# Optimization experiments

Hardware: AMD Instinct MI355X
Metric: run time of the kernel (lower is better)

## Reference

```python
import jax, jax.numpy as jnp
import numpy as np

N_ATOMS = 100000
N_CHANNELS = 4
N_EDGES = 6400000
SMEARING = 1.0


def setup_inputs() -> dict:
    key = jax.random.key(0)
    k1, k2, k3 = jax.random.split(key, 3)
    charges = jax.random.normal(k1, (N_ATOMS, N_CHANNELS), dtype=jnp.float32)
    neighbor_indices = jax.random.randint(k2, (N_EDGES, 2), 0, N_ATOMS, dtype=jnp.int64)
    # physical distances strictly positive, typical cutoff-range values
    neighbor_distances = jax.random.uniform(k3, (N_EDGES,), dtype=jnp.float32,
                                            minval=0.5, maxval=6.0)
    return {"charges": charges,
            "neighbor_indices": neighbor_indices,
            "neighbor_distances": neighbor_distances}


def reference(charges, neighbor_indices, neighbor_distances):
    # Short-range Coulomb potential: erfc(r / (sqrt(2)*smearing)) / r
    pot_bare = jax.scipy.special.erfc(
        neighbor_distances / (jnp.sqrt(jnp.float32(2.0)) * SMEARING)
    ) / neighbor_distances  # [E]

    atom_is = neighbor_indices[:, 0]
    atom_js = neighbor_indices[:, 1]

    contrib_is = charges[atom_js] * pot_bare[:, None]  # [E, C]
    potential = jnp.zeros_like(charges).at[atom_is].add(contrib_is)
    # half neighbor list (full_neighbor_list=False): symmetrize
    contrib_js = charges[atom_is] * pot_bare[:, None]
    potential = potential.at[atom_js].add(contrib_js)
    return potential / 2
```

## Files before the change

kernel.cpp:

```cpp
#include <hip/hip_runtime.h>
#include <hip/hip_fp16.h>

#define BLOCK 1024
#define NB_BIN 960
#define KCONS 48
#define RPB (NB_BIN / KCONS)
#define TILE_ATOMS 10000
#define NTILES_MAX 10
#define WPS_MAX 112
#define WPS_PAD 113
#define FB_TILE_ATOMS 10000
#define FB_TILE_FLOATS (FB_TILE_ATOMS * 2)
#define CPX 3
#define CHUNKS 24
#define RSQRT2 0.70710678118654752440f

typedef float v2f __attribute__((ext_vector_type(2)));
typedef unsigned long long ull;

__device__ __forceinline__ void atomic_add2(float* p, float a, float b) {
#if __has_builtin(__builtin_amdgcn_global_atomic_fadd_v2f32)
    v2f v = {a, b};
    __builtin_amdgcn_global_atomic_fadd_v2f32((v2f*)p, v);
#else
    unsafeAtomicAdd(p + 0, a);
    unsafeAtomicAdd(p + 1, b);
#endif
}

__device__ __forceinline__ void agent_store64(ull* p, ull v) {
    __hip_atomic_store(p, v, __ATOMIC_RELAXED, __HIP_MEMORY_SCOPE_AGENT);
}
__device__ __forceinline__ void agent_store32(unsigned int* p, unsigned int v) {
    __hip_atomic_store(p, v, __ATOMIC_RELAXED, __HIP_MEMORY_SCOPE_AGENT);
}

__device__ __forceinline__ float pot_half(float d) {
    float x = d * RSQRT2;
    float t = __builtin_amdgcn_rcpf(fmaf(0.3275911f, x, 1.0f));
    float p = fmaf(t, 0.5307027145f, -0.7265760135f);
    p = fmaf(t, p, 0.7107068705f);
    p = fmaf(t, p, -0.142248368f);
    p = fmaf(t, p, 0.127414796f);
    p *= t;
    return p * __expf(-0.5f * d * d) * __builtin_amdgcn_rcpf(d);
}

__global__ void detect_idx64_kernel(const unsigned int* __restrict__ idx_u32,
                                    int* __restrict__ flag) {
    __shared__ int nonzero;
    if (threadIdx.x == 0) nonzero = 0;
    __syncthreads();
    unsigned int v = idx_u32[2 * (threadIdx.x +   0) + 1]
                   | idx_u32[2 * (threadIdx.x + 256) + 1]
                   | idx_u32[2 * (threadIdx.x + 512) + 1]
                   | idx_u32[2 * (threadIdx.x + 768) + 1];
    if (v != 0u) atomicAdd(&nonzero, 1);
    __syncthreads();
    if (threadIdx.x == 0) *flag = (nonzero == 0) ? 1 : 0;
}


__global__ __launch_bounds__(BLOCK) void bin_kernel(
    const float4* __restrict__ charges, const void* __restrict__ idx,
    const float* __restrict__ dist,
    ull* __restrict__ entries, unsigned int* __restrict__ counts,
    float* __restrict__ out, const int* __restrict__ flag64,
    int n_edges, int nwords, int wps, int cap, int ntiles, int nb)
{
    __shared__ ull maskA[NTILES_MAX][WPS_PAD];
    __shared__ ull maskB[NTILES_MAX][WPS_PAD];
    __shared__ unsigned short wbase[NTILES_MAX][WPS_PAD];
    bool f64 = (*flag64 != 0);
    int b    = blockIdx.x;
    int lane = threadIdx.x & 63;
    int wave = threadIdx.x >> 6;
    ull lt = (1ull << lane) - 1ull;

    for (int wl = wave; wl < wps; wl += BLOCK / 64) {
        int gw = b * wps + wl;
        int ta = -1, tb = -1;
        if (gw < nwords) {
            int e = gw * 64 + lane;
            if (e < n_edges) {
                int a, bb;
                if (f64) { longlong2 w = ((const longlong2*)idx)[e]; a = (int)w.x; bb = (int)w.y; }
                else     { int2      w = ((const int2*)idx)[e];      a = w.x;      bb = w.y; }
                ta = a / TILE_ATOMS; tb = bb / TILE_ATOMS;
            }
        }
        for (int T = 0; T < ntiles; ++T) {
            ull ma = __ballot(ta == T);
            ull mb = __ballot(tb == T);
            if (lane == 0) { maskA[T][wl] = ma; maskB[T][wl] = mb; }
        }
    }
    __syncthreads();

    if ((int)threadIdx.x < ntiles) {
        int T = threadIdx.x;
        unsigned base = 0;
        for (int wl = 0; wl < wps; ++wl) {
            wbase[T][wl] = (unsigned short)base;
            base += (unsigned)(__popcll(maskA[T][wl]) + __popcll(maskB[T][wl]));
        }
        agent_store32(&counts[(size_t)T * nb + b],
                      base < (unsigned)cap ? base : (unsigned)cap);
    }
    __syncthreads();

    for (int wl = wave; wl < wps; wl += BLOCK / 64) {
        int gw = b * wps + wl;
        if (gw >= nwords) continue;
        int e = gw * 64 + lane;
        int a = 0, bb = 0, ta = -1, tb = -1;
        float q = 0.f;
        if (e < n_edges) {
            if (f64) { longlong2 w = ((const longlong2*)idx)[e]; a = (int)w.x; bb = (int)w.y; }
            else     { int2      w = ((const int2*)idx)[e];      a = w.x;      bb = w.y; }
            ta = a / TILE_ATOMS; tb = bb / TILE_ATOMS;
            q = pot_half(dist[e]);
        }
        ull qb = (ull)__float_as_uint(q) << 32;
        if (ta >= 0) {
            unsigned slot = wbase[ta][wl] + (unsigned)__popcll(maskA[ta][wl] & lt);
            ull* reg = entries + ((size_t)ta * nb + b) * cap;
            if (slot < (unsigned)cap) {
                unsigned lo = (unsigned)(a - ta * TILE_ATOMS) | ((unsigned)bb << 14);
                agent_store64(&reg[slot], qb | lo);
            } else {
                float4 g = charges[bb];
                float* o = out + (size_t)a * 4;
                unsafeAtomicAdd(o + 0, g.x * q); unsafeAtomicAdd(o + 1, g.y * q);
                unsafeAtomicAdd(o + 2, g.z * q); unsafeAtomicAdd(o + 3, g.w * q);
            }
        }
        if (tb >= 0) {
            unsigned slot = wbase[tb][wl] + (unsigned)__popcll(maskA[tb][wl])
                          + (unsigned)__popcll(maskB[tb][wl] & lt);
            ull* reg = entries + ((size_t)tb * nb + b) * cap;
            if (slot < (unsigned)cap) {
                unsigned lo = (unsigned)(bb - tb * TILE_ATOMS) | ((unsigned)a << 14);
                agent_store64(&reg[slot], qb | lo);
            } else {
                float4 g = charges[a];
                float* o = out + (size_t)bb * 4;
                unsafeAtomicAdd(o + 0, g.x * q); unsafeAtomicAdd(o + 1, g.y * q);
                unsafeAtomicAdd(o + 2, g.z * q); unsafeAtomicAdd(o + 3, g.w * q);
            }
        }
    }
}

__global__ __launch_bounds__(BLOCK, 8) void consume_pk(
    const float4* __restrict__ charges,
    const ull* __restrict__ entries, const unsigned int* __restrict__ counts,
    ull* __restrict__ partials, int cap, int nb, unsigned capmagic)
{
    __shared__ __half2 ht[TILE_ATOMS * 2];
    __shared__ unsigned cnts[RPB];
    int k = blockIdx.x % KCONS;
    int t = blockIdx.x / KCONS;
    for (int i = threadIdx.x; i < TILE_ATOMS * 2; i += BLOCK)
        ((unsigned*)ht)[i] = 0u;
    for (int r = threadIdx.x; r < RPB; r += BLOCK)
        cnts[r] = counts[(size_t)t * nb + k * RPB + r];
    __syncthreads();

    const ull* base = entries + ((size_t)t * nb + (size_t)k * RPB) * cap;
    int total = RPB * cap;
    for (int i0 = (int)threadIdx.x * 2; i0 < total; i0 += BLOCK * 2) {
        ulonglong2 e2 = *(const ulonglong2*)(base + i0);
        int r   = (int)(((ull)(unsigned)i0 * capmagic) >> 32);
        int pos = i0 - r * cap;
        unsigned cnt = cnts[r];
        #define PROC(EV)                                                     \
            { unsigned lo = (unsigned)(EV);                                  \
              int rel = lo & 16383; int other = (int)(lo >> 14);             \
              float q = __uint_as_float((unsigned)((EV) >> 32));             \
              float4 g = charges[other];                                     \
              __half2 h01 = __floats2half2_rn(g.x * q, g.y * q);             \
              __half2 h23 = __floats2half2_rn(g.z * q, g.w * q);             \
              unsafeAtomicAdd(&ht[rel * 2 + 0], h01);                        \
              unsafeAtomicAdd(&ht[rel * 2 + 1], h23); }
        if ((unsigned)pos     < cnt) PROC(e2.x)
        if ((unsigned)(pos+1) < cnt) PROC(e2.y)
        #undef PROC
    }
    __syncthreads();

    ull* pb = partials + (size_t)blockIdx.x * TILE_ATOMS;
    for (int r = threadIdx.x; r < TILE_ATOMS; r += BLOCK) {
        __half2 x0 = ht[r * 2 + 0], x1 = ht[r * 2 + 1];
        unsigned b0 = *(unsigned*)&x0, b1 = *(unsigned*)&x1;
        agent_store64(&pb[r], (ull)b0 | ((ull)b1 << 32));
    }
}

__global__ __launch_bounds__(256) void reduce_kernel(
    const ull* __restrict__ partials, float* __restrict__ out, int n_atoms)
{
    int a = blockIdx.x * 256 + threadIdx.x;
    if (a >= n_atoms) return;
    int t   = a / TILE_ATOMS;
    int rel = a - t * TILE_ATOMS;
    const ull* base = partials + ((size_t)t * KCONS) * TILE_ATOMS + rel;
    float4 s = make_float4(0.f, 0.f, 0.f, 0.f);
    #pragma unroll
    for (int k = 0; k < KCONS; ++k) {
        ull v = base[(size_t)k * TILE_ATOMS];
        s.x += __half2float(__ushort_as_half((unsigned short)( v        & 0xffff)));
        s.y += __half2float(__ushort_as_half((unsigned short)((v >> 16) & 0xffff)));
        s.z += __half2float(__ushort_as_half((unsigned short)((v >> 32) & 0xffff)));
        s.w += __half2float(__ushort_as_half((unsigned short)( v >> 48)));
    }
    float* o = out + (size_t)a * 4;
    atomic_add2(o + 0, s.x, s.y);
    atomic_add2(o + 2, s.z, s.w);
}


template <bool F64>
__device__ __forceinline__ void scan_chunk(
    const void* __restrict__ idx, const float* __restrict__ dist,
    const float2* __restrict__ charges2, float* __restrict__ tile,
    int tbase, int h, int e0, int e1)
{
    int ec = e0 + ((e1 - e0) & ~3);
    for (int e4 = e0 + (int)threadIdx.x * 4; e4 < ec; e4 += BLOCK * 4) {
        int a[4], b[4];
        if (F64) {
            #pragma unroll
            for (int k = 0; k < 4; ++k) {
                longlong2 w = ((const longlong2*)idx)[e4 + k];
                a[k] = (int)w.x; b[k] = (int)w.y;
            }
        } else {
            int4 w01 = ((const int4*)idx)[(e4 >> 1) + 0];
            int4 w23 = ((const int4*)idx)[(e4 >> 1) + 1];
            a[0] = w01.x; b[0] = w01.y; a[1] = w01.z; b[1] = w01.w;
            a[2] = w23.x; b[2] = w23.y; a[3] = w23.z; b[3] = w23.w;
        }
        float4 dv = *(const float4*)(dist + e4);
        float d[4] = {dv.x, dv.y, dv.z, dv.w};
        float q[4];
        #pragma unroll
        for (int k = 0; k < 4; ++k) q[k] = pot_half(d[k]);
        #pragma unroll
        for (int k = 0; k < 4; ++k) {
            unsigned ri = (unsigned)(a[k] - tbase);
            unsigned rj = (unsigned)(b[k] - tbase);
            if (ri < FB_TILE_ATOMS) {
                float2 g = charges2[b[k] * 2 + h];
                atomicAdd(&tile[ri * 2 + 0], g.x * q[k]);
                atomicAdd(&tile[ri * 2 + 1], g.y * q[k]);
            }
            if (rj < FB_TILE_ATOMS) {
                float2 g = charges2[a[k] * 2 + h];
                atomicAdd(&tile[rj * 2 + 0], g.x * q[k]);
                atomicAdd(&tile[rj * 2 + 1], g.y * q[k]);
            }
        }
    }
    for (int e = ec + (int)threadIdx.x; e < e1; e += BLOCK) {
        int a, b;
        if (F64) { longlong2 w = ((const longlong2*)idx)[e]; a = (int)w.x; b = (int)w.y; }
        else     { int2      w = ((const int2*)idx)[e];      a = w.x;      b = w.y; }
        unsigned ri = (unsigned)(a - tbase), rj = (unsigned)(b - tbase);
        if (ri < FB_TILE_ATOMS || rj < FB_TILE_ATOMS) {
            float q = pot_half(dist[e]);
            if (ri < FB_TILE_ATOMS) {
                float2 g = charges2[b * 2 + h];
                atomicAdd(&tile[ri * 2 + 0], g.x * q);
                atomicAdd(&tile[ri * 2 + 1], g.y * q);
            }
            if (rj < FB_TILE_ATOMS) {
                float2 g = charges2[a * 2 + h];
                atomicAdd(&tile[rj * 2 + 0], g.x * q);
                atomicAdd(&tile[rj * 2 + 1], g.y * q);
            }
        }
    }
}

__global__ __launch_bounds__(BLOCK, 8) void fused_tile_kernel(
    const float2* __restrict__ charges2, const void* __restrict__ idx,
    const float* __restrict__ dist, float* __restrict__ out,
    const int* __restrict__ flag64,
    int n_edges, int n_atoms, int ntiles, int epc)
{
    __shared__ float tile[FB_TILE_FLOATS];
    int x   = blockIdx.x & 7;
    int m   = blockIdx.x >> 3;
    int nth = ntiles * 2;
    int cw  = m / nth;
    int rem = m - cw * nth;
    int t   = rem >> 1;
    int h   = rem & 1;
    int c   = x * CPX + cw;
    int tbase = t * FB_TILE_ATOMS;
    for (int i = threadIdx.x; i < FB_TILE_FLOATS; i += BLOCK) tile[i] = 0.f;
    bool f64 = (*flag64 != 0);
    __syncthreads();

    int e0 = c * epc;
    int e1 = min(n_edges, e0 + epc);
    if (e0 < e1) {
        if (f64) scan_chunk<true >(idx, dist, charges2, tile, tbase, h, e0, e1);
        else     scan_chunk<false>(idx, dist, charges2, tile, tbase, h, e0, e1);
    }
    __syncthreads();

    const float2* src = (const float2*)tile;
    for (int r = threadIdx.x; r < FB_TILE_ATOMS; r += BLOCK) {
        int a = tbase + r;
        if (a >= n_atoms) break;
        float2 v = src[r];
        if (v.x != 0.f || v.y != 0.f)
            atomic_add2(out + (size_t)a * 4 + h * 2, v.x, v.y);
    }
}


extern "C" void kernel_launch(void* const* d_in, const int* in_sizes, int n_in,
                              void* d_out, int out_size, void* d_ws, size_t ws_size,
                              hipStream_t stream) {
    const float4* charges  = (const float4*)d_in[0];
    const float2* charges2 = (const float2*)d_in[0];
    const void*   idx      = d_in[1];
    const float*  dist     = (const float*)d_in[2];
    int n_edges = in_sizes[2];
    int n_atoms = in_sizes[0] / 4;
    int* flag   = (int*)d_ws;

    const size_t CTRL = 1024;
    int nwords = (n_edges + 63) / 64;
    int wps    = (nwords + NB_BIN - 1) / NB_BIN;
    int ntiles = (n_atoms + TILE_ATOMS - 1) / TILE_ATOMS;
    int slice  = wps * 64;
    int cap    = ((slice * 2 / (ntiles > 0 ? ntiles : 1)) * 115 / 100 + 63)
                 & ~63;
    unsigned capmagic = (unsigned)((0x100000000ull + cap - 1) / (unsigned)cap);
    size_t nreg           = (size_t)ntiles * NB_BIN;
    size_t counts_bytes   = (nreg * sizeof(unsigned int) + 255) & ~(size_t)255;
    size_t entries_bytes  = nreg * (size_t)cap * 8ull;
    size_t partials_bytes = (size_t)ntiles * KCONS * TILE_ATOMS * 8ull;
    size_t needed = CTRL + counts_bytes + entries_bytes + partials_bytes;
    bool use_binned = (ws_size >= needed) && (ntiles <= NTILES_MAX) &&
                      (wps <= WPS_MAX) && (n_atoms <= (1 << 17)) &&
                      (slice * 2 < 65536);

    (void)hipMemsetAsync(d_out, 0, (size_t)out_size * sizeof(float), stream);
    detect_idx64_kernel<<<1, 256, 0, stream>>>((const unsigned int*)idx, flag);

    if (use_binned) {
        unsigned int* counts = (unsigned int*)((char*)d_ws + CTRL);
        ull* entries  = (ull*)((char*)d_ws + CTRL + counts_bytes);
        ull* partials = (ull*)((char*)d_ws + CTRL + counts_bytes + entries_bytes);
        bin_kernel<<<NB_BIN, BLOCK, 0, stream>>>(
            charges, idx, dist, entries, counts, (float*)d_out, flag,
            n_edges, nwords, wps, cap, ntiles, NB_BIN);
        consume_pk<<<ntiles * KCONS, BLOCK, 0, stream>>>(
            charges, entries, counts, partials, cap, NB_BIN, capmagic);
        reduce_kernel<<<(n_atoms + 255) / 256, 256, 0, stream>>>(
            partials, (float*)d_out, n_atoms);
    } else {
        int ntiles_fb = (n_atoms + FB_TILE_ATOMS - 1) / FB_TILE_ATOMS;
        int epc = (((n_edges + CHUNKS - 1) / CHUNKS) + 3) & ~3;
        fused_tile_kernel<<<ntiles_fb * 2 * CHUNKS, BLOCK, 0, stream>>>(
            charges2, idx, dist, (float*)d_out, flag, n_edges, n_atoms,
            ntiles_fb, epc);
    }
}
```

Before: 232.2 us.

## Split binned entries into packed index array and fp16 potential array

The 64-bit binned entries (fp32 potential plus packed indices) become a 32-bit index array and a separate 16-bit half-precision potential array, which cuts intermediate traffic from 8 to 6 bytes per entry. The consumer now handles four entries per thread with vector loads and predicates invalid slots by zeroing q and clamping indices rather than branching. This saves memory bandwidth between the binning and consume kernels. In exchange the potential loses precision, and unused slots now trigger extra charge gathers and LDS atomics.

```diff
diff --git a/kernel.cpp b/kernel.cpp
--- a/kernel.cpp
+++ b/kernel.cpp
@@ -34,6 +34,9 @@
 __device__ __forceinline__ void agent_store32(unsigned int* p, unsigned int v) {
     __hip_atomic_store(p, v, __ATOMIC_RELAXED, __HIP_MEMORY_SCOPE_AGENT);
 }
+__device__ __forceinline__ void agent_store16(unsigned short* p, unsigned short v) {
+    __hip_atomic_store(p, v, __ATOMIC_RELAXED, __HIP_MEMORY_SCOPE_AGENT);
+}
 
 __device__ __forceinline__ float pot_half(float d) {
     float x = d * RSQRT2;
@@ -64,7 +67,8 @@
 __global__ __launch_bounds__(BLOCK) void bin_kernel(
     const float4* __restrict__ charges, const void* __restrict__ idx,
     const float* __restrict__ dist,
-    ull* __restrict__ entries, unsigned int* __restrict__ counts,
+    unsigned int* __restrict__ ro, unsigned short* __restrict__ qh,
+    unsigned int* __restrict__ counts,
     float* __restrict__ out, const int* __restrict__ flag64,
     int n_edges, int nwords, int wps, int cap, int ntiles, int nb)
 {
@@ -121,13 +125,14 @@
             ta = a / TILE_ATOMS; tb = bb / TILE_ATOMS;
             q = pot_half(dist[e]);
         }
-        ull qb = (ull)__float_as_uint(q) << 32;
+        unsigned short qf = __half_as_ushort(__float2half(q));
         if (ta >= 0) {
             unsigned slot = wbase[ta][wl] + (unsigned)__popcll(maskA[ta][wl] & lt);
-            ull* reg = entries + ((size_t)ta * nb + b) * cap;
+            size_t gs = ((size_t)ta * nb + b) * cap + slot;
             if (slot < (unsigned)cap) {
-                unsigned lo = (unsigned)(a - ta * TILE_ATOMS) | ((unsigned)bb << 14);
-                agent_store64(&reg[slot], qb | lo);
+                agent_store32(&ro[gs],
+                    (unsigned)(a - ta * TILE_ATOMS) | ((unsigned)bb << 14));
+                agent_store16(&qh[gs], qf);
             } else {
                 float4 g = charges[bb];
                 float* o = out + (size_t)a * 4;
@@ -138,10 +143,11 @@
         if (tb >= 0) {
             unsigned slot = wbase[tb][wl] + (unsigned)__popcll(maskA[tb][wl])
                           + (unsigned)__popcll(maskB[tb][wl] & lt);
-            ull* reg = entries + ((size_t)tb * nb + b) * cap;
+            size_t gs = ((size_t)tb * nb + b) * cap + slot;
             if (slot < (unsigned)cap) {
-                unsigned lo = (unsigned)(bb - tb * TILE_ATOMS) | ((unsigned)a << 14);
-                agent_store64(&reg[slot], qb | lo);
+                agent_store32(&ro[gs],
+                    (unsigned)(bb - tb * TILE_ATOMS) | ((unsigned)a << 14));
+                agent_store16(&qh[gs], qf);
             } else {
                 float4 g = charges[a];
                 float* o = out + (size_t)bb * 4;
@@ -154,8 +160,10 @@
 
 __global__ __launch_bounds__(BLOCK, 8) void consume_pk(
     const float4* __restrict__ charges,
-    const ull* __restrict__ entries, const unsigned int* __restrict__ counts,
-    ull* __restrict__ partials, int cap, int nb, unsigned capmagic)
+    const unsigned int* __restrict__ ro, const unsigned short* __restrict__ qh,
+    const unsigned int* __restrict__ counts,
+    ull* __restrict__ partials, int cap, int nb, unsigned capmagic,
+    int max_atom)
 {
     __shared__ __half2 ht[TILE_ATOMS * 2];
     __shared__ unsigned cnts[RPB];
@@ -167,24 +175,28 @@
         cnts[r] = counts[(size_t)t * nb + k * RPB + r];
     __syncthreads();
 
-    const ull* base = entries + ((size_t)t * nb + (size_t)k * RPB) * cap;
+    size_t rbase = ((size_t)t * nb + (size_t)k * RPB) * cap;
+    const unsigned int*   rb = ro + rbase;
+    const unsigned short* qb = qh + rbase;
     int total = RPB * cap;
-    for (int i0 = (int)threadIdx.x * 2; i0 < total; i0 += BLOCK * 2) {
-        ulonglong2 e2 = *(const ulonglong2*)(base + i0);
+    for (int i0 = (int)threadIdx.x * 4; i0 < total; i0 += BLOCK * 4) {
+        uint4 rr = *(const uint4*)(rb + i0);
+        ull   q4 = *(const ull*)(qb + i0);
         int r   = (int)(((ull)(unsigned)i0 * capmagic) >> 32);
         int pos = i0 - r * cap;
         unsigned cnt = cnts[r];
-        #define PROC(EV)                                                     \
-            { unsigned lo = (unsigned)(EV);                                  \
-              int rel = lo & 16383; int other = (int)(lo >> 14);             \
-              float q = __uint_as_float((unsigned)((EV) >> 32));             \
+        #define PROC(J, RO)                                                  \
+            { float q = ((unsigned)(pos + J) < cnt)                          \
+                  ? __half2float(__ushort_as_half(                           \
+                        (unsigned short)(q4 >> (16 * J)))) : 0.f;            \
+              int rel = min((int)((RO) & 16383u), TILE_ATOMS - 1);           \
+              int other = min((int)((RO) >> 14), max_atom);                  \
               float4 g = charges[other];                                     \
               __half2 h01 = __floats2half2_rn(g.x * q, g.y * q);             \
               __half2 h23 = __floats2half2_rn(g.z * q, g.w * q);             \
               unsafeAtomicAdd(&ht[rel * 2 + 0], h01);                        \
               unsafeAtomicAdd(&ht[rel * 2 + 1], h23); }
-        if ((unsigned)pos     < cnt) PROC(e2.x)
-        if ((unsigned)(pos+1) < cnt) PROC(e2.y)
+        PROC(0, rr.x) PROC(1, rr.y) PROC(2, rr.z) PROC(3, rr.w)
         #undef PROC
     }
     __syncthreads();
@@ -341,11 +353,12 @@
     int cap    = ((slice * 2 / (ntiles > 0 ? ntiles : 1)) * 115 / 100 + 63)
                  & ~63;
     unsigned capmagic = (unsigned)((0x100000000ull + cap - 1) / (unsigned)cap);
-    size_t nreg           = (size_t)ntiles * NB_BIN;
-    size_t counts_bytes   = (nreg * sizeof(unsigned int) + 255) & ~(size_t)255;
-    size_t entries_bytes  = nreg * (size_t)cap * 8ull;
+    size_t nslots         = (size_t)ntiles * NB_BIN * (size_t)cap;
+    size_t counts_bytes   = ((size_t)ntiles * NB_BIN * 4 + 255) & ~(size_t)255;
+    size_t ro_bytes       = (nslots * 4ull + 255) & ~(size_t)255;
+    size_t qh_bytes       = (nslots * 2ull + 255) & ~(size_t)255;
     size_t partials_bytes = (size_t)ntiles * KCONS * TILE_ATOMS * 8ull;
-    size_t needed = CTRL + counts_bytes + entries_bytes + partials_bytes;
+    size_t needed = CTRL + counts_bytes + ro_bytes + qh_bytes + partials_bytes;
     bool use_binned = (ws_size >= needed) && (ntiles <= NTILES_MAX) &&
                       (wps <= WPS_MAX) && (n_atoms <= (1 << 17)) &&
                       (slice * 2 < 65536);
@@ -354,14 +367,17 @@
     detect_idx64_kernel<<<1, 256, 0, stream>>>((const unsigned int*)idx, flag);
 
     if (use_binned) {
-        unsigned int* counts = (unsigned int*)((char*)d_ws + CTRL);
-        ull* entries  = (ull*)((char*)d_ws + CTRL + counts_bytes);
-        ull* partials = (ull*)((char*)d_ws + CTRL + counts_bytes + entries_bytes);
+        char* p = (char*)d_ws + CTRL;
+        unsigned int*   counts = (unsigned int*)p;   p += counts_bytes;
+        unsigned int*   ro     = (unsigned int*)p;   p += ro_bytes;
+        unsigned short* qh     = (unsigned short*)p; p += qh_bytes;
+        ull*            partials = (ull*)p;
         bin_kernel<<<NB_BIN, BLOCK, 0, stream>>>(
-            charges, idx, dist, entries, counts, (float*)d_out, flag,
+            charges, idx, dist, ro, qh, counts, (float*)d_out, flag,
             n_edges, nwords, wps, cap, ntiles, NB_BIN);
         consume_pk<<<ntiles * KCONS, BLOCK, 0, stream>>>(
-            charges, entries, counts, partials, cap, NB_BIN, capmagic);
+            charges, ro, qh, counts, partials, cap, NB_BIN, capmagic,
+            n_atoms - 1);
         reduce_kernel<<<(n_atoms + 255) / 256, 256, 0, stream>>>(
             partials, (float*)d_out, n_atoms);
     } else {
```

Measured after the change: 291.2 us. +25.4%, slower.
